# Performance work log

Hardware: AMD Instinct MI355X
Metric: run time of the kernel (lower is better)

## Reference

```python
import math
import jax, jax.numpy as jnp
import numpy as np

B, T, S, H, L, NH = 2, 512, 2048, 768, 32, 12
INTERMED = 4 * H


def _make_pe(max_len, hidden):
    position = np.arange(max_len)[:, None].astype(np.float32)
    div_term = np.exp(np.arange(0, hidden, 2).astype(np.float32) * (-math.log(10000.0) / hidden))
    pe = np.zeros((max_len, hidden), dtype=np.float32)
    pe[:, 0::2] = np.sin(position * div_term)
    pe[:, 1::2] = np.cos(position * div_term)
    return jnp.asarray(pe)


def setup_inputs() -> dict:
    key = jax.random.key(0)
    ks = jax.random.split(key, 10)
    token_reps = jax.random.normal(ks[0], (B, T, H), dtype=jnp.float32)
    starts = jax.random.randint(ks[1], (B, S), 0, T - L)
    lens = jax.random.randint(ks[2], (B, S), 1, L + 1)
    span_ids = jnp.stack([starts, starts + lens], axis=-1)  # (B,S,2)
    span_masks = jax.random.uniform(ks[3], (B, S)) > 0.2
    pe = _make_pe(T, H)
    dummy_query = jax.random.normal(ks[4], (H,), dtype=jnp.float32) * 0.02
    in_proj_w = jax.random.normal(ks[5], (3 * H, H), dtype=jnp.float32) * 0.02
    in_proj_b = jnp.zeros((3 * H,), jnp.float32)
    out_proj_w = jax.random.normal(ks[6], (H, H), dtype=jnp.float32) * 0.02
    out_proj_b = jnp.zeros((H,), jnp.float32)
    norm_g = jnp.ones((H,), jnp.float32)
    norm_b = jnp.zeros((H,), jnp.float32)
    ffn_w1 = jax.random.normal(ks[7], (INTERMED, H), dtype=jnp.float32) * (math.sqrt(2.0 / H))
    ffn_b1 = jnp.zeros((INTERMED,), jnp.float32)
    ffn_w2 = jax.random.normal(ks[8], (H, INTERMED), dtype=jnp.float32) * (math.sqrt(2.0 / INTERMED))
    ffn_b2 = jnp.zeros((H,), jnp.float32)
    return dict(token_reps=token_reps, span_ids=span_ids, span_masks=span_masks,
                pooling=0, pe=pe, dummy_query=dummy_query,
                in_proj_w=in_proj_w, in_proj_b=in_proj_b,
                out_proj_w=out_proj_w, out_proj_b=out_proj_b,
                norm_g=norm_g, norm_b=norm_b,
                ffn_w1=ffn_w1, ffn_b1=ffn_b1, ffn_w2=ffn_w2, ffn_b2=ffn_b2)


def _layernorm(x, g, b, eps=1e-5):
    mu = jnp.mean(x, axis=-1, keepdims=True)
    var = jnp.mean(jnp.square(x - mu), axis=-1, keepdims=True)
    return (x - mu) * jax.lax.rsqrt(var + eps) * g + b


def reference(token_reps, span_ids, span_masks, pooling, pe, dummy_query,
              in_proj_w, in_proj_b, out_proj_w, out_proj_b,
              norm_g, norm_b, ffn_w1, ffn_b1, ffn_w2, ffn_b2):
    b, t, h = token_reps.shape
    s = span_ids.shape[1]
    hd = h // NH
    # positional encoding over the sequence (dropout=0 / eval mode)
    x = token_reps + pe[:t]
    # ragged -> padded gather of span tokens
    starts = span_ids[..., 0]
    lens = (span_ids[..., 1] - starts) * span_masks.astype(span_ids.dtype)  # (B,S)
    ar = jnp.arange(L)
    pos = starts[..., None] + ar                     # (B,S,L)
    valid = ar[None, None, :] < lens[..., None]      # (B,S,L) True = real token
    idx = jnp.clip(pos, 0, t - 1)
    gathered = jax.vmap(lambda xb, ib: xb[ib])(x, idx)   # (B,S,L,H)
    gathered = gathered * valid[..., None]
    # guard fully-masked rows (masked-out / zero-len spans): keep one key valid,
    # output is zeroed at the end anyway (matches torch span_reps[~mask]=0)
    any_v = jnp.any(valid, axis=-1)
    valid = valid.at[..., 0].set(valid[..., 0] | ~any_v)
    # single-query multi-head attention (torch nn.MultiheadAttention math)
    Wq, Wk, Wv = jnp.split(in_proj_w, 3, axis=0)
    bq, bk, bv = jnp.split(in_proj_b, 3, axis=0)
    q = (dummy_query @ Wq.T + bq).reshape(NH, hd)                  # (NH,hd)
    k = (gathered @ Wk.T + bk).reshape(b, s, L, NH, hd)
    v = (gathered @ Wv.T + bv).reshape(b, s, L, NH, hd)
    scores = jnp.einsum('nd,bslnd->bsnl', q, k) / math.sqrt(hd)    # (B,S,NH,L)
    scores = jnp.where(valid[:, :, None, :], scores, -jnp.inf)
    attn = jax.nn.softmax(scores, axis=-1)
    ctx = jnp.einsum('bsnl,bslnd->bsnd', attn, v).reshape(b, s, h)
    attn_out = ctx @ out_proj_w.T + out_proj_b
    # residual + LayerNorm, FFN, residual + same LayerNorm
    x1 = _layernorm(attn_out + dummy_query, norm_g, norm_b)
    ffn = jax.nn.relu(x1 @ ffn_w1.T + ffn_b1) @ ffn_w2.T + ffn_b2
    out = _layernorm(ffn + x1, norm_g, norm_b)
    out = out * span_masks[..., None]
    return out
```

## Files before the change

### kernel.cpp

```cpp
#include <hip/hip_runtime.h>
#include <math.h>

static constexpr int B_  = 2;
static constexpr int T_  = 512;
static constexpr int S_  = 2048;
static constexpr int H_  = 768;
static constexpr int L_  = 32;
static constexpr int NH_ = 12;
static constexpr int HD_ = 64;
static constexpr int IM_ = 3072;

typedef __bf16 bf16x8 __attribute__((ext_vector_type(8)));
typedef float  f32x4  __attribute__((ext_vector_type(4)));

__device__ __forceinline__ float bf2f(unsigned short u) {
    return __uint_as_float(((unsigned)u) << 16);
}
__device__ __forceinline__ unsigned short f2bf(float f) {
    unsigned u = __float_as_uint(f);
    u += 0x7fffu + ((u >> 16) & 1u);
    return (unsigned short)(u >> 16);
}
__device__ __forceinline__ void gl_lds16(const void* g, void* l) {
    __builtin_amdgcn_global_load_lds((const __attribute__((address_space(1))) void*)g,
                                     (__attribute__((address_space(3))) void*)l, 16, 0, 0);
}

__global__ void k_mask(const int* __restrict__ raw, int* __restrict__ mout) {
    __shared__ int bad;
    if (threadIdx.x == 0) bad = 0;
    __syncthreads();
    int v = raw[threadIdx.x];
    if (v != 0 && v != 1) bad = 1;
    __syncthreads();
    int byte_layout = bad;
    const unsigned char* rb = (const unsigned char*)raw;
    for (int i = threadIdx.x; i < B_ * S_; i += 1024)
        mout[i] = byte_layout ? (int)rb[i] : raw[i];
}

__global__ void k_q(const float* __restrict__ dq, const float* __restrict__ w,
                    const float* __restrict__ b, float* __restrict__ q) {
    int wv = threadIdx.x >> 6, lane = threadIdx.x & 63;
    int i = blockIdx.x * 4 + wv;
    const float* row = w + (size_t)i * H_;
    float acc = 0.f;
#pragma unroll
    for (int k = 0; k < 12; ++k) acc += dq[lane + 64 * k] * row[lane + 64 * k];
    for (int m = 32; m; m >>= 1) acc += __shfl_xor(acc, m, 64);
    if (lane == 0) q[i] = acc + b[i];
}

__global__ void k_wqeff(const float* __restrict__ q, const float* __restrict__ w,
                        float* __restrict__ wq) {
    int i = blockIdx.x * 256 + threadIdx.x;
    if (i >= NH_ * H_) return;
    int n = i / H_, hh = i % H_;
    float acc = 0.f;
    for (int d = 0; d < HD_; ++d)
        acc += q[n * HD_ + d] * w[(size_t)(H_ + n * HD_ + d) * H_ + hh];
    wq[i] = acc;
}

__global__ void k_castw(const float* __restrict__ s0, const float* __restrict__ s1,
                        const float* __restrict__ s2, const float* __restrict__ s3,
                        unsigned short* __restrict__ d0, unsigned short* __restrict__ d1,
                        unsigned short* __restrict__ d2, unsigned short* __restrict__ d3) {
    const long n0 = (long)H_ * H_, n2 = (long)IM_ * H_;
    long gid = (long)(blockIdx.x * 256 + threadIdx.x) * 8;
    const float* s; unsigned short* d; long off;
    if (gid < n0)                { s = s0; d = d0; off = gid; }
    else if (gid < 2 * n0)       { s = s1; d = d1; off = gid - n0; }
    else if (gid < 2 * n0 + n2)  { s = s2; d = d2; off = gid - 2 * n0; }
    else                         { s = s3; d = d3; off = gid - 2 * n0 - n2; }
    float4 f0 = *(const float4*)(s + off);
    float4 f1 = *(const float4*)(s + off + 4);
    uint4 o;
    o.x = (unsigned)f2bf(f0.x) | ((unsigned)f2bf(f0.y) << 16);
    o.y = (unsigned)f2bf(f0.z) | ((unsigned)f2bf(f0.w) << 16);
    o.z = (unsigned)f2bf(f1.x) | ((unsigned)f2bf(f1.y) << 16);
    o.w = (unsigned)f2bf(f1.z) | ((unsigned)f2bf(f1.w) << 16);
    *(uint4*)(d + off) = o;
}

__global__ void k_addpe(const float* __restrict__ tr, const float* __restrict__ pe,
                        unsigned short* __restrict__ x) {
    int i = (blockIdx.x * 256 + threadIdx.x) * 8;
    if (i >= B_ * T_ * H_) return;
    float4 a0 = *(const float4*)(tr + i);
    float4 a1 = *(const float4*)(tr + i + 4);
    const float* pp = pe + (i % (T_ * H_));
    float4 p0 = *(const float4*)pp;
    float4 p1 = *(const float4*)(pp + 4);
    uint4 o;
    o.x = (unsigned)f2bf(a0.x + p0.x) | ((unsigned)f2bf(a0.y + p0.y) << 16);
    o.y = (unsigned)f2bf(a0.z + p0.z) | ((unsigned)f2bf(a0.w + p0.w) << 16);
    o.z = (unsigned)f2bf(a1.x + p1.x) | ((unsigned)f2bf(a1.y + p1.y) << 16);
    o.w = (unsigned)f2bf(a1.z + p1.z) | ((unsigned)f2bf(a1.w + p1.w) << 16);
    *(uint4*)(x + i) = o;
}

__global__ void k_stok(const unsigned short* __restrict__ x, const float* __restrict__ wq,
                       float* __restrict__ stok) {
    int bt = blockIdx.x;
    int lane = threadIdx.x & 63, w = threadIdx.x >> 6;
    const unsigned short* xr = x + (size_t)bt * H_;
    float xv[12];
#pragma unroll
    for (int k = 0; k < 12; ++k) xv[k] = bf2f(xr[lane + 64 * k]);
#pragma unroll
    for (int hh = 0; hh < 3; ++hh) {
        int n = w * 3 + hh;
        const float* wr = wq + (size_t)n * H_;
        float acc = 0.f;
#pragma unroll
        for (int k = 0; k < 12; ++k) acc += xv[k] * wr[lane + 64 * k];
        for (int m = 32; m; m >>= 1) acc += __shfl_xor(acc, m, 64);
        if (lane == 0) stok[bt * NH_ + n] = acc;
    }
}

template <bool RELU, bool OBF>
__global__ __launch_bounds__(256)
void gemm_bt(const unsigned short* __restrict__ A, const unsigned short* __restrict__ W,
             const float* __restrict__ bias, void* __restrict__ Cout,
             int M, int N, int K) {
    __shared__ unsigned short As[2 * 8192];
    __shared__ unsigned short Bs[2 * 8192];
    const int bm = blockIdx.y * 128, bn = blockIdx.x * 128;
    const int tid = threadIdx.x, lane = tid & 63, wid = tid >> 6;
    const int wm = (wid >> 1) * 64, wn = (wid & 1) * 64;
    const int r8 = lane >> 3, c8 = lane & 7;
    const int swc = (c8 ^ r8) * 8;
    const unsigned short* agp = A + (size_t)(bm + wid * 32 + r8) * K + swc;
    const unsigned short* bgp = W + (size_t)(bn + wid * 32 + r8) * K + swc;
    unsigned short* lA = As + wid * 2048;
    unsigned short* lB = Bs + wid * 2048;

    f32x4 acc[4][4];
#pragma unroll
    for (int i = 0; i < 4; ++i)
#pragma unroll
        for (int j = 0; j < 4; ++j) acc[i][j] = f32x4{0.f, 0.f, 0.f, 0.f};

    const int mrow = lane & 15;
    const int l7 = lane & 7;
    const int cq0 = lane >> 4;
    const int NIT = K >> 6;

#pragma unroll
    for (int p = 0; p < 2; ++p) {
        const int k0 = p << 6;
        const int lo = p * 8192;
#pragma unroll
        for (int j = 0; j < 4; ++j) {
            gl_lds16(agp + (size_t)(8 * j) * K + k0, lA + lo + j * 512);
            gl_lds16(bgp + (size_t)(8 * j) * K + k0, lB + lo + j * 512);
        }
    }

    for (int it = 0; it < NIT; ++it) {
        if (it < NIT - 1) asm volatile("s_waitcnt vmcnt(8)" ::: "memory");
        else              asm volatile("s_waitcnt vmcnt(0)" ::: "memory");
        asm volatile("s_barrier" ::: "memory");
        const int lo = (it & 1) * 8192;
        const unsigned short* cA = As + lo;
        const unsigned short* cB = Bs + lo;
        bf16x8 af[2][4], bfr[2][4];
#pragma unroll
        for (int s = 0; s < 2; ++s) {
            const int cq = s * 4 + cq0;
            const int sw = (cq ^ l7) * 8;
#pragma unroll
            for (int i = 0; i < 4; ++i)
                af[s][i] = *(const bf16x8*)(cA + (wm + i * 16 + mrow) * 64 + sw);
#pragma unroll
            for (int j = 0; j < 4; ++j)
                bfr[s][j] = *(const bf16x8*)(cB + (wn + j * 16 + mrow) * 64 + sw);
        }
#pragma unroll
        for (int s = 0; s < 2; ++s)
#pragma unroll
            for (int i = 0; i < 4; ++i)
#pragma unroll
                for (int j = 0; j < 4; ++j)
                    acc[i][j] = __builtin_amdgcn_mfma_f32_16x16x32_bf16(af[s][i], bfr[s][j], acc[i][j], 0, 0, 0);
        asm volatile("s_barrier" ::: "memory");
        if (it + 2 < NIT) {
            const int k0 = (it + 2) << 6;
#pragma unroll
            for (int j = 0; j < 4; ++j) {
                gl_lds16(agp + (size_t)(8 * j) * K + k0, lA + lo + j * 512);
                gl_lds16(bgp + (size_t)(8 * j) * K + k0, lB + lo + j * 512);
            }
        }
    }

    const int lr = (lane >> 4) * 4, lc = lane & 15;
#pragma unroll
    for (int j = 0; j < 4; ++j) {
        int col = bn + wn + j * 16 + lc;
        float bv = bias[col];
#pragma unroll
        for (int i = 0; i < 4; ++i) {
            int row0 = bm + wm + i * 16 + lr;
#pragma unroll
            for (int r = 0; r < 4; ++r) {
                float v = acc[i][j][r] + bv;
                if (RELU) v = fmaxf(v, 0.f);
                if (OBF)
                    ((unsigned short*)Cout)[(size_t)(row0 + r) * N + col] = f2bf(v);
                else
                    ((float*)Cout)[(size_t)(row0 + r) * N + col] = v;
            }
        }
    }
}

__global__ void k_attn(const float* __restrict__ stok, const unsigned short* __restrict__ vtok,
                       const int* __restrict__ span_ids, const int* __restrict__ masks,
                       unsigned short* __restrict__ ctx) {
    int r = blockIdx.x, b = r / S_;
    unsigned short* out = ctx + (size_t)r * H_;
    int tid = threadIdx.x;
    __shared__ float w[NH_][L_];
    __shared__ int idxs[L_];
    __shared__ int s_len;
    if (tid == 0) {
        int m = masks[r];
        int st = span_ids[2 * r], en = span_ids[2 * r + 1];
        int len = m ? (en - st) : 0;
        len = len < 0 ? 0 : (len > L_ ? L_ : len);
        s_len = len;
    }
    __syncthreads();
    int len = s_len;
    if (len == 0) {
        for (int h2 = tid; h2 < H_ / 2; h2 += 256) ((unsigned*)out)[h2] = 0u;
        return;
    }
    if (tid < L_) {
        int p = span_ids[2 * r] + tid;
        idxs[tid] = p < 0 ? 0 : (p > T_ - 1 ? T_ - 1 : p);
    }
    __syncthreads();
    for (int i = tid; i < NH_ * L_; i += 256) {
        int n = i / L_, l = i % L_;
        w[n][l] = (l < len) ? stok[(size_t)(b * T_ + idxs[l]) * NH_ + n] * 0.125f : -INFINITY;
    }
    __syncthreads();
    if (tid < NH_) {
        float mx = -INFINITY;
        for (int l = 0; l < len; ++l) mx = fmaxf(mx, w[tid][l]);
        float sum = 0.f;
        for (int l = 0; l < len; ++l) { float e = __expf(w[tid][l] - mx); w[tid][l] = e; sum += e; }
        float inv = 1.f / sum;
        for (int l = 0; l < len; ++l) w[tid][l] *= inv;
    }
    __syncthreads();
    if (tid < 192) {
        int h0 = tid * 4, n = h0 >> 6;
        float a0 = 0.f, a1 = 0.f, a2 = 0.f, a3 = 0.f;
        for (int l = 0; l < len; ++l) {
            float wl = w[n][l];
            const unsigned short* vr = vtok + (size_t)(b * T_ + idxs[l]) * H_ + h0;
            uint2 u = *(const uint2*)vr;
            a0 += wl * bf2f((unsigned short)(u.x & 0xffff));
            a1 += wl * bf2f((unsigned short)(u.x >> 16));
            a2 += wl * bf2f((unsigned short)(u.y & 0xffff));
            a3 += wl * bf2f((unsigned short)(u.y >> 16));
        }
        uint2 o;
        o.x = (unsigned)f2bf(a0) | ((unsigned)f2bf(a1) << 16);
        o.y = (unsigned)f2bf(a2) | ((unsigned)f2bf(a3) << 16);
        *(uint2*)(out + h0) = o;
    }
}

__global__ void k_ln(const float* __restrict__ inp, const float* __restrict__ res,
                     const float* __restrict__ g, const float* __restrict__ bt,
                     float* __restrict__ outp, unsigned short* __restrict__ outbf,
                     const int* __restrict__ masks, int res_broadcast, int apply_mask) {
    int r = blockIdx.x;
    const float* irow = inp + (size_t)r * H_;
    const float* rrow = res_broadcast ? res : res + (size_t)r * H_;
    float* orow = outp + (size_t)r * H_;
    int tid = threadIdx.x;
    float v[3];
    float lsum = 0.f;
#pragma unroll
    for (int i = 0; i < 3; ++i) {
        int h = tid + 256 * i;
        v[i] = irow[h] + rrow[h];
        lsum += v[i];
    }
    __shared__ float sh[256];
    sh[tid] = lsum;
    __syncthreads();
    for (int st = 128; st > 0; st >>= 1) {
        if (tid < st) sh[tid] += sh[tid + st];
        __syncthreads();
    }
    float mean = sh[0] * (1.f / H_);
    __syncthreads();
    float lvar = 0.f;
#pragma unroll
    for (int i = 0; i < 3; ++i) { float d = v[i] - mean; lvar += d * d; }
    sh[tid] = lvar;
    __syncthreads();
    for (int st = 128; st > 0; st >>= 1) {
        if (tid < st) sh[tid] += sh[tid + st];
        __syncthreads();
    }
    float var = sh[0] * (1.f / H_);
    float scale = rsqrtf(var + 1e-5f);
    float mfac = apply_mask ? (masks[r] ? 1.f : 0.f) : 1.f;
#pragma unroll
    for (int i = 0; i < 3; ++i) {
        int h = tid + 256 * i;
        float o = ((v[i] - mean) * scale * g[h] + bt[h]) * mfac;
        orow[h] = o;
        if (outbf) outbf[(size_t)r * H_ + h] = f2bf(o);
    }
}

extern "C" void kernel_launch(void* const* d_in, const int* in_sizes, int n_in,
                              void* d_out, int out_size, void* d_ws, size_t ws_size,
                              hipStream_t stream) {
    const float* token_reps = (const float*)d_in[0];
    const int*   span_ids   = (const int*)d_in[1];
    const int*   masks_raw  = (const int*)d_in[2];
    const float* pe   = (const float*)d_in[4];
    const float* dq   = (const float*)d_in[5];
    const float* in_w = (const float*)d_in[6];
    const float* in_b = (const float*)d_in[7];
    const float* ow   = (const float*)d_in[8];
    const float* ob   = (const float*)d_in[9];
    const float* g    = (const float*)d_in[10];
    const float* bt   = (const float*)d_in[11];
    const float* w1   = (const float*)d_in[12];
    const float* b1   = (const float*)d_in[13];
    const float* w2   = (const float*)d_in[14];
    const float* b2   = (const float*)d_in[15];

    const int BS = B_ * S_;
    const int BT = B_ * T_;

    float* fws   = (float*)d_ws;
    float* stok  = fws;
    float* qv    = stok + BT * NH_;
    float* wqeff = qv + H_;
    float* A1    = wqeff + NH_ * H_;
    float* x1f   = A1 + (size_t)BS * H_;
    unsigned short* us   = (unsigned short*)(x1f + (size_t)BS * H_);
    unsigned short* xbf  = us;
    unsigned short* vtok = xbf + (size_t)BT * H_;
    unsigned short* ctx  = vtok + (size_t)BT * H_;
    unsigned short* x1bf = ctx + (size_t)BS * H_;
    unsigned short* f1   = x1bf + (size_t)BS * H_;
    unsigned short* wvb  = f1 + (size_t)BS * IM_;
    unsigned short* owb  = wvb + H_ * H_;
    unsigned short* w1b  = owb + H_ * H_;
    unsigned short* w2b  = w1b + IM_ * H_;
    int* maskn = (int*)(w2b + H_ * IM_);
    float* f2 = A1;

    k_mask<<<1, 1024, 0, stream>>>(masks_raw, maskn);
    k_q<<<H_ / 4, 256, 0, stream>>>(dq, in_w, in_b, qv);
    k_wqeff<<<(NH_ * H_ + 255) / 256, 256, 0, stream>>>(qv, in_w, wqeff);
    {
        long total8 = ((long)2 * H_ * H_ + (long)2 * IM_ * H_) / 8;
        k_castw<<<(int)(total8 / 256), 256, 0, stream>>>(
            in_w + (size_t)2 * H_ * H_, ow, w1, w2, wvb, owb, w1b, w2b);
    }
    k_addpe<<<(BT * H_ / 8 + 255) / 256, 256, 0, stream>>>(token_reps, pe, xbf);
    k_stok<<<BT, 256, 0, stream>>>(xbf, wqeff, stok);
    {
        dim3 grid(H_ / 128, BT / 128);
        gemm_bt<false, true><<<grid, 256, 0, stream>>>(xbf, wvb, in_b + 2 * H_, vtok, BT, H_, H_);
    }
    k_attn<<<BS, 256, 0, stream>>>(stok, vtok, span_ids, maskn, ctx);
    {
        dim3 grid(H_ / 128, BS / 128);
        gemm_bt<false, false><<<grid, 256, 0, stream>>>(ctx, owb, ob, A1, BS, H_, H_);
    }
    k_ln<<<BS, 256, 0, stream>>>(A1, dq, g, bt, x1f, x1bf, nullptr, 1, 0);
    {
        dim3 grid(IM_ / 128, BS / 128);
        gemm_bt<true, true><<<grid, 256, 0, stream>>>(x1bf, w1b, b1, f1, BS, IM_, H_);
    }
    {
        dim3 grid(H_ / 128, BS / 128);
        gemm_bt<false, false><<<grid, 256, 0, stream>>>(f1, w2b, b2, f2, BS, H_, IM_);
    }
    k_ln<<<BS, 256, 0, stream>>>(f2, x1f, g, bt, (float*)d_out, nullptr, maskn, 0, 1);
}
```

Baseline: 271.1 us.

## Add split-K with atomic accumulation to small-N GEMMs and drop double buffering

Adds a split-K mode to the GEMM: for the value projection, out-projection and FFN down-projection, the grid gains a z-dimension of 4 K-slices whose partial results are combined with float atomicAdd into zeroed buffers. This raises block count for the N=768 GEMMs that otherwise launch few workgroups. The value projection now writes fp32 and needs an extra cast kernel to bf16, and extra memsets are added. The GEMM's two-stage LDS double-buffered prefetch pipeline is replaced by a single buffer with synchronous load and sync each iteration, which removes load/compute overlap for all GEMMs, including the large FFN up-projection, and atomics add memory traffic.

```diff
diff --git a/kernel.cpp b/kernel.cpp
--- a/kernel.cpp
+++ b/kernel.cpp
@@ -83,6 +83,19 @@
     *(uint4*)(d + off) = o;
 }
 
+__global__ void k_castv(const float* __restrict__ src, unsigned short* __restrict__ dst, int n) {
+    int i = (blockIdx.x * 256 + threadIdx.x) * 8;
+    if (i >= n) return;
+    float4 f0 = *(const float4*)(src + i);
+    float4 f1 = *(const float4*)(src + i + 4);
+    uint4 o;
+    o.x = (unsigned)f2bf(f0.x) | ((unsigned)f2bf(f0.y) << 16);
+    o.y = (unsigned)f2bf(f0.z) | ((unsigned)f2bf(f0.w) << 16);
+    o.z = (unsigned)f2bf(f1.x) | ((unsigned)f2bf(f1.y) << 16);
+    o.w = (unsigned)f2bf(f1.z) | ((unsigned)f2bf(f1.w) << 16);
+    *(uint4*)(dst + i) = o;
+}
+
 __global__ void k_addpe(const float* __restrict__ tr, const float* __restrict__ pe,
                         unsigned short* __restrict__ x) {
     int i = (blockIdx.x * 256 + threadIdx.x) * 8;
@@ -120,20 +133,21 @@
     }
 }
 
-template <bool RELU, bool OBF>
+template <bool RELU, bool OBF, bool ATOMIC>
 __global__ __launch_bounds__(256)
 void gemm_bt(const unsigned short* __restrict__ A, const unsigned short* __restrict__ W,
              const float* __restrict__ bias, void* __restrict__ Cout,
-             int M, int N, int K) {
-    __shared__ unsigned short As[2 * 8192];
-    __shared__ unsigned short Bs[2 * 8192];
+             int M, int N, int K, int kLen) {
+    __shared__ unsigned short As[8192];
+    __shared__ unsigned short Bs[8192];
     const int bm = blockIdx.y * 128, bn = blockIdx.x * 128;
+    const int kOff = blockIdx.z * kLen;
     const int tid = threadIdx.x, lane = tid & 63, wid = tid >> 6;
     const int wm = (wid >> 1) * 64, wn = (wid & 1) * 64;
     const int r8 = lane >> 3, c8 = lane & 7;
     const int swc = (c8 ^ r8) * 8;
-    const unsigned short* agp = A + (size_t)(bm + wid * 32 + r8) * K + swc;
-    const unsigned short* bgp = W + (size_t)(bn + wid * 32 + r8) * K + swc;
+    const unsigned short* agp = A + (size_t)(bm + wid * 32 + r8) * K + kOff + swc;
+    const unsigned short* bgp = W + (size_t)(bn + wid * 32 + r8) * K + kOff + swc;
     unsigned short* lA = As + wid * 2048;
     unsigned short* lB = Bs + wid * 2048;
 
@@ -146,26 +160,16 @@
     const int mrow = lane & 15;
     const int l7 = lane & 7;
     const int cq0 = lane >> 4;
-    const int NIT = K >> 6;
-
-#pragma unroll
-    for (int p = 0; p < 2; ++p) {
-        const int k0 = p << 6;
-        const int lo = p * 8192;
+    const int NIT = kLen >> 6;
+
+    for (int it = 0; it < NIT; ++it) {
+        const int k0 = it << 6;
 #pragma unroll
         for (int j = 0; j < 4; ++j) {
-            gl_lds16(agp + (size_t)(8 * j) * K + k0, lA + lo + j * 512);
-            gl_lds16(bgp + (size_t)(8 * j) * K + k0, lB + lo + j * 512);
+            gl_lds16(agp + (size_t)(8 * j) * K + k0, lA + j * 512);
+            gl_lds16(bgp + (size_t)(8 * j) * K + k0, lB + j * 512);
         }
-    }
-
-    for (int it = 0; it < NIT; ++it) {
-        if (it < NIT - 1) asm volatile("s_waitcnt vmcnt(8)" ::: "memory");
-        else              asm volatile("s_waitcnt vmcnt(0)" ::: "memory");
-        asm volatile("s_barrier" ::: "memory");
-        const int lo = (it & 1) * 8192;
-        const unsigned short* cA = As + lo;
-        const unsigned short* cB = Bs + lo;
+        __syncthreads();
         bf16x8 af[2][4], bfr[2][4];
 #pragma unroll
         for (int s = 0; s < 2; ++s) {
@@ -173,10 +177,10 @@
             const int sw = (cq ^ l7) * 8;
 #pragma unroll
             for (int i = 0; i < 4; ++i)
-                af[s][i] = *(const bf16x8*)(cA + (wm + i * 16 + mrow) * 64 + sw);
+                af[s][i] = *(const bf16x8*)(As + (wm + i * 16 + mrow) * 64 + sw);
 #pragma unroll
             for (int j = 0; j < 4; ++j)
-                bfr[s][j] = *(const bf16x8*)(cB + (wn + j * 16 + mrow) * 64 + sw);
+                bfr[s][j] = *(const bf16x8*)(Bs + (wn + j * 16 + mrow) * 64 + sw);
         }
 #pragma unroll
         for (int s = 0; s < 2; ++s)
@@ -185,22 +189,15 @@
 #pragma unroll
                 for (int j = 0; j < 4; ++j)
                     acc[i][j] = __builtin_amdgcn_mfma_f32_16x16x32_bf16(af[s][i], bfr[s][j], acc[i][j], 0, 0, 0);
-        asm volatile("s_barrier" ::: "memory");
-        if (it + 2 < NIT) {
-            const int k0 = (it + 2) << 6;
-#pragma unroll
-            for (int j = 0; j < 4; ++j) {
-                gl_lds16(agp + (size_t)(8 * j) * K + k0, lA + lo + j * 512);
-                gl_lds16(bgp + (size_t)(8 * j) * K + k0, lB + lo + j * 512);
-            }
-        }
-    }
-
+        __syncthreads();
+    }
+
+    const bool addb = !ATOMIC || blockIdx.z == 0;
     const int lr = (lane >> 4) * 4, lc = lane & 15;
 #pragma unroll
     for (int j = 0; j < 4; ++j) {
         int col = bn + wn + j * 16 + lc;
-        float bv = bias[col];
+        float bv = addb ? bias[col] : 0.f;
 #pragma unroll
         for (int i = 0; i < 4; ++i) {
             int row0 = bm + wm + i * 16 + lr;
@@ -208,7 +205,9 @@
             for (int r = 0; r < 4; ++r) {
                 float v = acc[i][j][r] + bv;
                 if (RELU) v = fmaxf(v, 0.f);
-                if (OBF)
+                if (ATOMIC)
+                    atomicAdd(&((float*)Cout)[(size_t)(row0 + r) * N + col], v);
+                else if (OBF)
                     ((unsigned short*)Cout)[(size_t)(row0 + r) * N + col] = f2bf(v);
                 else
                     ((float*)Cout)[(size_t)(row0 + r) * N + col] = v;
@@ -352,7 +351,8 @@
     float* wqeff = qv + H_;
     float* A1    = wqeff + NH_ * H_;
     float* x1f   = A1 + (size_t)BS * H_;
-    unsigned short* us   = (unsigned short*)(x1f + (size_t)BS * H_);
+    float* vtokf = x1f + (size_t)BS * H_;
+    unsigned short* us   = (unsigned short*)(vtokf + (size_t)BT * H_);
     unsigned short* xbf  = us;
     unsigned short* vtok = xbf + (size_t)BT * H_;
     unsigned short* ctx  = vtok + (size_t)BT * H_;
@@ -365,6 +365,8 @@
     int* maskn = (int*)(w2b + H_ * IM_);
     float* f2 = A1;
 
+    hipMemsetAsync(vtokf, 0, (size_t)BT * H_ * 4, stream);
+    hipMemsetAsync(A1, 0, (size_t)BS * H_ * 4, stream);
     k_mask<<<1, 1024, 0, stream>>>(masks_raw, maskn);
     k_q<<<H_ / 4, 256, 0, stream>>>(dq, in_w, in_b, qv);
     k_wqeff<<<(NH_ * H_ + 255) / 256, 256, 0, stream>>>(qv, in_w, wqeff);
@@ -376,22 +378,28 @@
     k_addpe<<<(BT * H_ / 8 + 255) / 256, 256, 0, stream>>>(token_reps, pe, xbf);
     k_stok<<<BT, 256, 0, stream>>>(xbf, wqeff, stok);
     {
-        dim3 grid(H_ / 128, BT / 128);
-        gemm_bt<false, true><<<grid, 256, 0, stream>>>(xbf, wvb, in_b + 2 * H_, vtok, BT, H_, H_);
+        dim3 grid(H_ / 128, BT / 128, 4);
+        gemm_bt<false, false, true><<<grid, 256, 0, stream>>>(
+            xbf, wvb, in_b + 2 * H_, vtokf, BT, H_, H_, H_ / 4);
+        k_castv<<<(BT * H_ / 8 + 255) / 256, 256, 0, stream>>>(vtokf, vtok, BT * H_);
     }
     k_attn<<<BS, 256, 0, stream>>>(stok, vtok, span_ids, maskn, ctx);
     {
-        dim3 grid(H_ / 128, BS / 128);
-        gemm_bt<false, false><<<grid, 256, 0, stream>>>(ctx, owb, ob, A1, BS, H_, H_);
+        dim3 grid(H_ / 128, BS / 128, 4);
+        gemm_bt<false, false, true><<<grid, 256, 0, stream>>>(
+            ctx, owb, ob, A1, BS, H_, H_, H_ / 4);
     }
     k_ln<<<BS, 256, 0, stream>>>(A1, dq, g, bt, x1f, x1bf, nullptr, 1, 0);
+    hipMemsetAsync(f2, 0, (size_t)BS * H_ * 4, stream);
     {
-        dim3 grid(IM_ / 128, BS / 128);
-        gemm_bt<true, true><<<grid, 256, 0, stream>>>(x1bf, w1b, b1, f1, BS, IM_, H_);
+        dim3 grid(IM_ / 128, BS / 128, 1);
+        gemm_bt<true, true, false><<<grid, 256, 0, stream>>>(
+            x1bf, w1b, b1, f1, BS, IM_, H_, H_);
     }
     {
-        dim3 grid(H_ / 128, BS / 128);
-        gemm_bt<false, false><<<grid, 256, 0, stream>>>(f1, w2b, b2, f2, BS, H_, IM_);
+        dim3 grid(H_ / 128, BS / 128, 4);
+        gemm_bt<false, false, true><<<grid, 256, 0, stream>>>(
+            f1, w2b, b2, f2, BS, H_, IM_, IM_ / 4);
     }
     k_ln<<<BS, 256, 0, stream>>>(f2, x1f, g, bt, (float*)d_out, nullptr, maskn, 0, 1);
 }
```

Result: slower. 327.7 us (+20.9%).
